# Performance work log

Hardware: AMD Instinct MI355X
Metric: run time of the kernel (lower is better)

Reference implementation:

```python
import jax, jax.numpy as jnp
import numpy as np

N_NODES = 50000
N_EDGES = 600000
D_IN = 128
D_OUT = 128
EPS = 0.0  # PyG GINConv default eps


def setup_inputs() -> dict:
    key = jax.random.key(0)
    k1, k2, k3 = jax.random.split(key, 3)
    x = jax.random.normal(k1, (N_NODES, D_IN), dtype=jnp.float32)
    edge_index = jax.random.randint(k2, (2, N_EDGES), 0, N_NODES, dtype=jnp.int64)
    W = jax.random.normal(k3, (D_OUT, D_IN), dtype=jnp.float32) * 0.02  # torch Linear weight [out, in]
    b = jnp.zeros((D_OUT,), dtype=jnp.float32)
    return {"x": x, "edge_index": edge_index, "W": W, "b": b}


def reference(x, edge_index, W, b):
    src = edge_index[0]  # message source nodes
    dst = edge_index[1]  # aggregation targets
    # sum-aggregate neighbor features: agg_i = sum_{(j->i) in E} x_j
    agg = jax.ops.segment_sum(x[src], dst, num_segments=x.shape[0])
    h = (1.0 + EPS) * x + agg
    # nn.Linear: h @ W^T + b
    return jnp.einsum('nd,od->no', h, W) + b
```

## Files before the change

### kernel.cpp

```cpp
#include <hip/hip_runtime.h>

#define D 128
#define LDW 136
#define BM 64
#define CAP 64

typedef __attribute__((ext_vector_type(8))) short bf16x8;
typedef __attribute__((ext_vector_type(4))) float f32x4;

static __device__ __forceinline__ ushort f2bf(float f) {
    union { float f; unsigned u; } c; c.f = f;
    unsigned u = c.u;
    return (ushort)((u + 0x7fffu + ((u >> 16) & 1u)) >> 16);
}
static __device__ __forceinline__ float bflo(unsigned v) {
    union { unsigned u; float f; } c; c.u = v << 16; return c.f;
}
static __device__ __forceinline__ float bfhi(unsigned v) {
    union { unsigned u; float f; } c; c.u = v & 0xffff0000u; return c.f;
}

__global__ __launch_bounds__(256) void gin_prep0(const float* __restrict__ W,
                                                 ushort* __restrict__ Wb, int w4,
                                                 int* __restrict__ deg, int ndeg4) {
    int stride = gridDim.x * 256;
    int tid0 = blockIdx.x * 256 + threadIdx.x;
    for (int i = tid0; i < ndeg4; i += stride)
        ((int4*)deg)[i] = make_int4(0, 0, 0, 0);
    for (int i = tid0; i < w4; i += stride) {
        float4 v = ((const float4*)W)[i];
        ushort4 o;
        o.x = f2bf(v.x); o.y = f2bf(v.y); o.z = f2bf(v.z); o.w = f2bf(v.w);
        ((ushort4*)Wb)[i] = o;
    }
}

__global__ __launch_bounds__(256) void gin_hist_cvt(const float* __restrict__ x,
                                                    ushort* __restrict__ xb, int n4,
                                                    const int* __restrict__ src,
                                                    const int* __restrict__ dst,
                                                    int* __restrict__ deg,
                                                    int* __restrict__ bucket, int nedges) {
    int stride = gridDim.x * 256;
    int tid0 = blockIdx.x * 256 + threadIdx.x;
    for (int i = tid0; i < n4; i += stride) {
        float4 v = ((const float4*)x)[i];
        ushort4 o;
        o.x = f2bf(v.x); o.y = f2bf(v.y); o.z = f2bf(v.z); o.w = f2bf(v.w);
        ((ushort4*)xb)[i] = o;
    }
    for (int e = tid0; e < nedges; e += stride) {
        int d = dst[e];
        int slot = atomicAdd(&deg[d], 1);
        if (slot < CAP) bucket[(size_t)d * CAP + slot] = src[e];
    }
}

__global__ __launch_bounds__(1024) void gin_fused16(const ushort* __restrict__ xb,
                                                    const int* __restrict__ deg,
                                                    const int* __restrict__ bucket,
                                                    const ushort* __restrict__ Wb,
                                                    const float* __restrict__ bias,
                                                    float* __restrict__ out, int nnodes) {
    __shared__ ushort Wl[D * LDW];
    __shared__ ushort Al[BM * LDW];

    int tid = threadIdx.x;
    int base = blockIdx.x * BM;

    for (int i = tid; i < D * D / 8; i += 1024) {
        uint4 v = ((const uint4*)Wb)[i];
        int row = i >> 4;
        int col = (i & 15) * 8;
        *(uint4*)&Wl[row * LDW + col] = v;
    }

    {
        int w = tid >> 6, lane = tid & 63;
        const unsigned* xbu = (const unsigned*)xb;
        for (int t = 0; t < 4; ++t) {
            int row = w * 4 + t;
            int node = base + row;
            unsigned ov = 0;
            if (node < nnodes) {
                int dcnt = deg[node];
                if (dcnt > CAP) dcnt = CAP;
                const int* lst = bucket + (size_t)node * CAP;
                unsigned sv = xbu[(size_t)node * 64 + lane];
                float2 acc;
                acc.x = bflo(sv);
                acc.y = bfhi(sv);
                int e = 0;
                for (; e + 8 <= dcnt; e += 8) {
                    int s0 = lst[e],     s1 = lst[e + 1];
                    int s2 = lst[e + 2], s3 = lst[e + 3];
                    int s4 = lst[e + 4], s5 = lst[e + 5];
                    int s6 = lst[e + 6], s7 = lst[e + 7];
                    unsigned v0 = xbu[(size_t)s0 * 64 + lane];
                    unsigned v1 = xbu[(size_t)s1 * 64 + lane];
                    unsigned v2 = xbu[(size_t)s2 * 64 + lane];
                    unsigned v3 = xbu[(size_t)s3 * 64 + lane];
                    unsigned v4 = xbu[(size_t)s4 * 64 + lane];
                    unsigned v5 = xbu[(size_t)s5 * 64 + lane];
                    unsigned v6 = xbu[(size_t)s6 * 64 + lane];
                    unsigned v7 = xbu[(size_t)s7 * 64 + lane];
                    acc.x += ((bflo(v0) + bflo(v1)) + (bflo(v2) + bflo(v3)))
                           + ((bflo(v4) + bflo(v5)) + (bflo(v6) + bflo(v7)));
                    acc.y += ((bfhi(v0) + bfhi(v1)) + (bfhi(v2) + bfhi(v3)))
                           + ((bfhi(v4) + bfhi(v5)) + (bfhi(v6) + bfhi(v7)));
                }
                if (e + 4 <= dcnt) {
                    int s0 = lst[e],     s1 = lst[e + 1];
                    int s2 = lst[e + 2], s3 = lst[e + 3];
                    unsigned v0 = xbu[(size_t)s0 * 64 + lane];
                    unsigned v1 = xbu[(size_t)s1 * 64 + lane];
                    unsigned v2 = xbu[(size_t)s2 * 64 + lane];
                    unsigned v3 = xbu[(size_t)s3 * 64 + lane];
                    acc.x += (bflo(v0) + bflo(v1)) + (bflo(v2) + bflo(v3));
                    acc.y += (bfhi(v0) + bfhi(v1)) + (bfhi(v2) + bfhi(v3));
                    e += 4;
                }
                for (; e < dcnt; ++e) {
                    unsigned v = xbu[(size_t)lst[e] * 64 + lane];
                    acc.x += bflo(v);
                    acc.y += bfhi(v);
                }
                ov = (unsigned)f2bf(acc.x) | ((unsigned)f2bf(acc.y) << 16);
            }
            *(unsigned*)&Al[row * LDW + lane * 2] = ov;
        }
    }
    __syncthreads();

    int w = tid >> 6, l = tid & 63;
    int wr = w >> 2, wc = w & 3;
    int lr = l & 15, hi = l >> 4;

    f32x4 acc[2];
    acc[0] = (f32x4)0.0f;
    acc[1] = (f32x4)0.0f;

#pragma unroll
    for (int ks = 0; ks < 4; ks++) {
        int kof = ks * 32 + hi * 8;
        bf16x8 a = *(bf16x8*)&Al[(wr * 16 + lr) * LDW + kof];
#pragma unroll
        for (int t = 0; t < 2; t++) {
            bf16x8 bm = *(bf16x8*)&Wl[(wc * 32 + t * 16 + lr) * LDW + kof];
            acc[t] = __builtin_amdgcn_mfma_f32_16x16x32_bf16(a, bm, acc[t], 0, 0, 0);
        }
    }

#pragma unroll
    for (int t = 0; t < 2; t++) {
        int col = wc * 32 + t * 16 + lr;
        float bv = bias[col];
#pragma unroll
        for (int rr = 0; rr < 4; rr++) {
            int row = base + wr * 16 + hi * 4 + rr;
            if (row < nnodes) out[(size_t)row * D + col] = acc[t][rr] + bv;
        }
    }
}

extern "C" void kernel_launch(void* const* d_in, const int* in_sizes, int n_in,
                              void* d_out, int out_size, void* d_ws, size_t ws_size,
                              hipStream_t stream) {
    const float* x  = (const float*)d_in[0];
    const int*   ei = (const int*)d_in[1];
    const float* W  = (const float*)d_in[2];
    const float* bb = (const float*)d_in[3];
    float* out = (float*)d_out;

    int nnodes = in_sizes[0] / D;
    int nedges = in_sizes[1] / 2;
    const int* srcp = ei;
    const int* dstp = ei + nedges;

    int nb = (nnodes + 255) / 256;
    int npad = nb * 256;

    char* p = (char*)d_ws;
    int* deg    = (int*)p;  p += (size_t)npad * 4;
    int* bucket = (int*)p;  p += (size_t)nnodes * CAP * 4;
    p = (char*)(((uintptr_t)p + 15) & ~(uintptr_t)15);
    ushort* xb = (ushort*)p; p += (size_t)nnodes * D * 2;
    ushort* Wb = (ushort*)p; p += (size_t)D * D * 2;

    int n4 = nnodes * (D / 4);
    int w4 = D * D / 4;
    int ndeg4 = npad / 4;
    int eb = (nedges + 255) / 256;

    gin_prep0<<<256, 256, 0, stream>>>(W, Wb, w4, deg, ndeg4);

    gin_hist_cvt<<<eb, 256, 0, stream>>>(x, xb, n4, srcp, dstp, deg, bucket, nedges);

    int gemb = (nnodes + BM - 1) / BM;
    gin_fused16<<<gemb, 1024, 0, stream>>>(xb, deg, bucket, Wb, bb, out, nnodes);
}
```

Before: 83.85 us.

## Transpose neighbor bucket to slot-major layout and store indices as ushort

The per-node neighbor bucket moves from node-major [node][slot] to slot-major [slot][node] layout, and source indices are stored as 16-bit when the node count fits. In the gather kernel each wave still handles one node at a time, so the index reads become strided by nnodes rather than contiguous, while in the histogram kernel atomic-slot writes for nearby destinations become more scattered. The aim is a smaller index footprint and less write traffic. The cost is a possible loss of locality on index reads.

After: 84.80 us. Within noise of the previous version (+1.1%).

```diff
diff --git a/kernel.cpp b/kernel.cpp
--- a/kernel.cpp
+++ b/kernel.cpp
@@ -35,12 +35,14 @@
     }
 }
 
+template<typename IT>
 __global__ __launch_bounds__(256) void gin_hist_cvt(const float* __restrict__ x,
                                                     ushort* __restrict__ xb, int n4,
                                                     const int* __restrict__ src,
                                                     const int* __restrict__ dst,
                                                     int* __restrict__ deg,
-                                                    int* __restrict__ bucket, int nedges) {
+                                                    IT* __restrict__ bucket,
+                                                    int nedges, int nnodes) {
     int stride = gridDim.x * 256;
     int tid0 = blockIdx.x * 256 + threadIdx.x;
     for (int i = tid0; i < n4; i += stride) {
@@ -52,16 +54,18 @@
     for (int e = tid0; e < nedges; e += stride) {
         int d = dst[e];
         int slot = atomicAdd(&deg[d], 1);
-        if (slot < CAP) bucket[(size_t)d * CAP + slot] = src[e];
-    }
-}
-
+        if (slot < CAP) bucket[(size_t)slot * nnodes + d] = (IT)src[e];
+    }
+}
+
+template<typename IT>
 __global__ __launch_bounds__(1024) void gin_fused16(const ushort* __restrict__ xb,
                                                     const int* __restrict__ deg,
-                                                    const int* __restrict__ bucket,
+                                                    const IT* __restrict__ bucket,
                                                     const ushort* __restrict__ Wb,
                                                     const float* __restrict__ bias,
-                                                    float* __restrict__ out, int nnodes) {
+                                                    float* __restrict__ out,
+                                                    int nnodes) {
     __shared__ ushort Wl[D * LDW];
     __shared__ ushort Al[BM * LDW];
 
@@ -85,17 +89,22 @@
             if (node < nnodes) {
                 int dcnt = deg[node];
                 if (dcnt > CAP) dcnt = CAP;
-                const int* lst = bucket + (size_t)node * CAP;
+                const IT* lst = bucket + node;
                 unsigned sv = xbu[(size_t)node * 64 + lane];
                 float2 acc;
                 acc.x = bflo(sv);
                 acc.y = bfhi(sv);
                 int e = 0;
                 for (; e + 8 <= dcnt; e += 8) {
-                    int s0 = lst[e],     s1 = lst[e + 1];
-                    int s2 = lst[e + 2], s3 = lst[e + 3];
-                    int s4 = lst[e + 4], s5 = lst[e + 5];
-                    int s6 = lst[e + 6], s7 = lst[e + 7];
+                    const IT* lb = lst + (size_t)e * nnodes;
+                    int s0 = (int)lb[0];
+                    int s1 = (int)lb[(size_t)1 * nnodes];
+                    int s2 = (int)lb[(size_t)2 * nnodes];
+                    int s3 = (int)lb[(size_t)3 * nnodes];
+                    int s4 = (int)lb[(size_t)4 * nnodes];
+                    int s5 = (int)lb[(size_t)5 * nnodes];
+                    int s6 = (int)lb[(size_t)6 * nnodes];
+                    int s7 = (int)lb[(size_t)7 * nnodes];
                     unsigned v0 = xbu[(size_t)s0 * 64 + lane];
                     unsigned v1 = xbu[(size_t)s1 * 64 + lane];
                     unsigned v2 = xbu[(size_t)s2 * 64 + lane];
@@ -110,8 +119,11 @@
                            + ((bfhi(v4) + bfhi(v5)) + (bfhi(v6) + bfhi(v7)));
                 }
                 if (e + 4 <= dcnt) {
-                    int s0 = lst[e],     s1 = lst[e + 1];
-                    int s2 = lst[e + 2], s3 = lst[e + 3];
+                    const IT* lb = lst + (size_t)e * nnodes;
+                    int s0 = (int)lb[0];
+                    int s1 = (int)lb[(size_t)1 * nnodes];
+                    int s2 = (int)lb[(size_t)2 * nnodes];
+                    int s3 = (int)lb[(size_t)3 * nnodes];
                     unsigned v0 = xbu[(size_t)s0 * 64 + lane];
                     unsigned v1 = xbu[(size_t)s1 * 64 + lane];
                     unsigned v2 = xbu[(size_t)s2 * 64 + lane];
@@ -121,7 +133,8 @@
                     e += 4;
                 }
                 for (; e < dcnt; ++e) {
-                    unsigned v = xbu[(size_t)lst[e] * 64 + lane];
+                    int s = (int)lst[(size_t)e * nnodes];
+                    unsigned v = xbu[(size_t)s * 64 + lane];
                     acc.x += bflo(v);
                     acc.y += bfhi(v);
                 }
@@ -179,10 +192,11 @@
 
     int nb = (nnodes + 255) / 256;
     int npad = nb * 256;
+    bool u16ok = (nnodes <= 65536);
 
     char* p = (char*)d_ws;
     int* deg    = (int*)p;  p += (size_t)npad * 4;
-    int* bucket = (int*)p;  p += (size_t)nnodes * CAP * 4;
+    void* bucket = (void*)p; p += (size_t)nnodes * CAP * (u16ok ? 2 : 4);
     p = (char*)(((uintptr_t)p + 15) & ~(uintptr_t)15);
     ushort* xb = (ushort*)p; p += (size_t)nnodes * D * 2;
     ushort* Wb = (ushort*)p; p += (size_t)D * D * 2;
@@ -191,11 +205,19 @@
     int w4 = D * D / 4;
     int ndeg4 = npad / 4;
     int eb = (nedges + 255) / 256;
+    int gemb = (nnodes + BM - 1) / BM;
 
     gin_prep0<<<256, 256, 0, stream>>>(W, Wb, w4, deg, ndeg4);
 
-    gin_hist_cvt<<<eb, 256, 0, stream>>>(x, xb, n4, srcp, dstp, deg, bucket, nedges);
-
-    int gemb = (nnodes + BM - 1) / BM;
-    gin_fused16<<<gemb, 1024, 0, stream>>>(xb, deg, bucket, Wb, bb, out, nnodes);
-}
+    if (u16ok) {
+        gin_hist_cvt<ushort><<<eb, 256, 0, stream>>>(x, xb, n4, srcp, dstp, deg,
+                                                     (ushort*)bucket, nedges, nnodes);
+        gin_fused16<ushort><<<gemb, 1024, 0, stream>>>(xb, deg, (const ushort*)bucket,
+                                                       Wb, bb, out, nnodes);
+    } else {
+        gin_hist_cvt<int><<<eb, 256, 0, stream>>>(x, xb, n4, srcp, dstp, deg,
+                                                  (int*)bucket, nedges, nnodes);
+        gin_fused16<int><<<gemb, 1024, 0, stream>>>(xb, deg, (const int*)bucket,
+                                                    Wb, bb, out, nnodes);
+    }
+}
```
